# Performance work log

Measured on AMD Instinct MI355X. Metric: run time of the kernel, lower is better.

## Reference

```python
import jax, jax.numpy as jnp
import numpy as np

N_NODES, N_EDGES, N_GRAPHS = 50000, 600000, 64
SEQ_DIM, HID = 384, 128


def setup_inputs() -> dict:
    key = jax.random.key(0)
    ks = jax.random.split(key, 12)
    inp = {}
    inp["seq_emb"] = jax.random.normal(ks[0], (N_GRAPHS, SEQ_DIM), jnp.float32)
    inp["node_x"] = jax.random.normal(ks[1], (N_NODES, SEQ_DIM), jnp.float32)
    inp["edge_index"] = jax.random.randint(ks[2], (2, N_EDGES), 0, N_NODES, dtype=jnp.int32)
    inp["node_batch"] = jnp.sort(jax.random.randint(ks[3], (N_NODES,), 0, N_GRAPHS, dtype=jnp.int32))
    # learned parameters (fan-in scaled)
    inp["W1"] = jax.random.normal(ks[4], (SEQ_DIM, HID), jnp.float32) / np.sqrt(SEQ_DIM)
    inp["b1"] = jnp.zeros((HID,), jnp.float32)
    inp["W2"] = jax.random.normal(ks[5], (HID, HID), jnp.float32) / np.sqrt(HID)
    inp["b2"] = jnp.zeros((HID,), jnp.float32)
    inp["Wf"] = jax.random.normal(ks[6], (SEQ_DIM + HID, 128), jnp.float32) / np.sqrt(SEQ_DIM + HID)
    inp["bf"] = jnp.zeros((128,), jnp.float32)
    inp["Wtp"] = jax.random.normal(ks[7], (128, 2), jnp.float32) / np.sqrt(128)
    inp["btp"] = jnp.zeros((2,), jnp.float32)
    inp["Wp"] = jax.random.normal(ks[8], (128, 1), jnp.float32) / np.sqrt(128)
    inp["bp"] = jnp.zeros((1,), jnp.float32)
    return inp


def _gcn_conv(x, W, b, src, dst, norm, n_nodes):
    # PyG GCNConv: out = A_hat @ (x W) + b, A_hat = D^-1/2 (A+I) D^-1/2
    h = x @ W                                   # [N, H]
    msg = h[src] * norm[:, None]                # [E+N, H] gather + scale
    return jax.ops.segment_sum(msg, dst, num_segments=n_nodes) + b


def reference(seq_emb, node_x, edge_index, node_batch,
              W1, b1, W2, b2, Wf, bf, Wtp, btp, Wp, bp):
    n = node_x.shape[0]
    b_graphs = seq_emb.shape[0]
    loops = jnp.arange(n, dtype=edge_index.dtype)
    src = jnp.concatenate([edge_index[0], loops])
    dst = jnp.concatenate([edge_index[1], loops])
    # symmetric normalization with self-loops (deg >= 1)
    deg = jax.ops.segment_sum(jnp.ones_like(dst, dtype=node_x.dtype), dst, num_segments=n)
    dinv = deg ** -0.5
    norm = dinv[src] * dinv[dst]

    g = jax.nn.relu(_gcn_conv(node_x, W1, b1, src, dst, norm, n))
    g = jax.nn.relu(_gcn_conv(g, W2, b2, src, dst, norm, n))

    # global mean pool over graphs
    sums = jax.ops.segment_sum(g, node_batch, num_segments=b_graphs)
    cnts = jax.ops.segment_sum(jnp.ones((n,), g.dtype), node_batch, num_segments=b_graphs)
    pooled = sums / jnp.maximum(cnts, 1.0)[:, None]

    fused = jax.nn.relu(jnp.concatenate([seq_emb, pooled], axis=1) @ Wf + bf)
    tp_logits = fused @ Wtp + btp
    prom_pred = fused @ Wp + bp
    return (tp_logits, prom_pred)
```

## Files before the change

kernel.cpp:

```cpp
#include <hip/hip_runtime.h>


#define HID 128

typedef __attribute__((ext_vector_type(8))) short bf16x8;
typedef __attribute__((ext_vector_type(4))) short bf16x4;
typedef __attribute__((ext_vector_type(4))) float f32x4;

static __device__ __forceinline__ short f2bf(float f) {
  union { float f; unsigned u; } v; v.f = f;
  unsigned r = v.u + 0x7fff + ((v.u >> 16) & 1);
  return (short)(r >> 16);
}
static __device__ __forceinline__ float bf2f(short s) {
  union { unsigned u; float f; } v;
  v.u = ((unsigned)(unsigned short)s) << 16;
  return v.f;
}

__global__ __launch_bounds__(256) void prep_w_k(const float* __restrict__ W1,
                                                short* __restrict__ W1t,
                                                const float* __restrict__ W2,
                                                short* __restrict__ W2t,
                                                int* __restrict__ deg, int N) {
  int idx = blockIdx.x * 256 + threadIdx.x;
  if (idx < 384 * HID) {
    int k = idx >> 7;
    int c = idx & 127;
    W1t[(size_t)c * 384 + k] = f2bf(W1[idx]);
  } else if (idx < 384 * HID + HID * HID) {
    int j = idx - 384 * HID;
    int k = j >> 7;
    int c = j & 127;
    W2t[(size_t)c * HID + k] = f2bf(W2[j]);
  }
  if (idx < N) deg[idx] = 0;
}

__global__ __launch_bounds__(256) void hist_k(const int* __restrict__ dst,
                                              int* __restrict__ cnt, int E) {
  int i = blockIdx.x * 256 + threadIdx.x;
  if (i < E) atomicAdd(&cnt[dst[i]], 1);
}

__global__ __launch_bounds__(256) void scan_bsum(const int* __restrict__ cnt,
                                                 int* __restrict__ bsum,
                                                 float* __restrict__ dinv, int n) {
  __shared__ int sm[256];
  int i = blockIdx.x * 256 + threadIdx.x;
  int v = (i < n) ? cnt[i] : 0;
  if (i < n) dinv[i] = rsqrtf((float)(v + 1));
  sm[threadIdx.x] = v;
  __syncthreads();
  for (int off = 128; off > 0; off >>= 1) {
    if (threadIdx.x < off) sm[threadIdx.x] += sm[threadIdx.x + off];
    __syncthreads();
  }
  if (threadIdx.x == 0) bsum[blockIdx.x] = sm[0];
}

__global__ __launch_bounds__(256) void scan_offsets(const int* __restrict__ cnt,
                                                    const int* __restrict__ bsum,
                                                    int* __restrict__ offs,
                                                    int* __restrict__ cur,
                                                    float* __restrict__ sums,
                                                    int nsum, int n, int nb) {
  __shared__ int sm[256];
  int t = threadIdx.x;
  int bid = blockIdx.x;
  int zi = bid * 256 + t;
  if (zi < nsum) sums[zi] = 0.f;
  int bv = (t < nb) ? bsum[t] : 0;
  sm[t] = bv;
  __syncthreads();
  for (int off = 1; off < 256; off <<= 1) {
    int add = (t >= off) ? sm[t - off] : 0;
    __syncthreads();
    sm[t] += add;
    __syncthreads();
  }
  int base = (bid > 0) ? sm[bid - 1] : 0;
  __syncthreads();
  int i = bid * 256 + t;
  int v = (i < n) ? cnt[i] : 0;
  sm[t] = v;
  __syncthreads();
  for (int off = 1; off < 256; off <<= 1) {
    int add = (t >= off) ? sm[t - off] : 0;
    __syncthreads();
    sm[t] += add;
    __syncthreads();
  }
  if (i < n) {
    offs[i] = base + sm[t] - v;
    cur[i] = 0;
  }
  if (i == n - 1) offs[n] = base + sm[t];
}

__global__ __launch_bounds__(256) void fill_k(const int* __restrict__ src,
                                              const int* __restrict__ dst,
                                              const int* __restrict__ offs,
                                              int* __restrict__ cur,
                                              int* __restrict__ csr, int E) {
  int i = blockIdx.x * 256 + threadIdx.x;
  if (i >= E) return;
  int d = dst[i];
  int p = offs[d] + atomicAdd(&cur[d], 1);
  csr[p] = src[i];
}

__global__ __launch_bounds__(256) void mfma_gemm1_k(const float* __restrict__ Af,
                                                    const short* __restrict__ Wt,
                                                    const float* __restrict__ scale,
                                                    short* __restrict__ C, int M) {
  constexpr int K = 384;
  constexpr int BK = 64;
  constexpr int ROWE = BK + 8;
  __shared__ short As[64 * ROWE];
  __shared__ short Bs[128 * ROWE];
  __shared__ float dln[64];

  const int tid = threadIdx.x;
  const int wave = tid >> 6;
  const int lane = tid & 63;
  const int l15 = lane & 15;
  const int lk = lane >> 4;
  const int mh = (wave >> 1) * 32;
  const int nh = (wave & 1) * 64;
  const int row0 = blockIdx.x * 64;

  if (tid < 64) {
    int r = row0 + tid;
    dln[tid] = (r < M) ? scale[r] : 0.f;
  }

  f32x4 acc[2][4] = {};

  for (int k0 = 0; k0 < K; k0 += BK) {
    __syncthreads();
#pragma unroll
    for (int it = 0; it < 4; ++it) {
      int f = tid + it * 256;
      int r = f >> 4;
      int kc = (f & 15) << 2;
      int gr = row0 + r;
      float4 v = make_float4(0.f, 0.f, 0.f, 0.f);
      if (gr < M) v = *(const float4*)&Af[(size_t)gr * K + k0 + kc];
      bf16x4 s;
      s[0] = f2bf(v.x); s[1] = f2bf(v.y); s[2] = f2bf(v.z); s[3] = f2bf(v.w);
      *(bf16x4*)&As[r * ROWE + kc] = s;
    }
#pragma unroll
    for (int it = 0; it < 4; ++it) {
      int f = tid + it * 256;
      int r = f >> 3;
      int kc = (f & 7) << 3;
      *(bf16x8*)&Bs[r * ROWE + kc] =
          *(const bf16x8*)&Wt[(size_t)r * K + k0 + kc];
    }
    __syncthreads();
#pragma unroll
    for (int ks = 0; ks < 2; ++ks) {
      bf16x8 af[2], bfr[4];
#pragma unroll
      for (int mf = 0; mf < 2; ++mf)
        af[mf] = *(const bf16x8*)&As[(mh + mf * 16 + l15) * ROWE + ks * 32 + lk * 8];
#pragma unroll
      for (int nf = 0; nf < 4; ++nf)
        bfr[nf] = *(const bf16x8*)&Bs[(nh + nf * 16 + l15) * ROWE + ks * 32 + lk * 8];
#pragma unroll
      for (int mf = 0; mf < 2; ++mf)
#pragma unroll
        for (int nf = 0; nf < 4; ++nf)
          acc[mf][nf] = __builtin_amdgcn_mfma_f32_16x16x32_bf16(
              af[mf], bfr[nf], acc[mf][nf], 0, 0, 0);
    }
  }
#pragma unroll
  for (int mf = 0; mf < 2; ++mf) {
#pragma unroll
    for (int r = 0; r < 4; ++r) {
      int lr = mh + mf * 16 + lk * 4 + r;
      int gr = row0 + lr;
      if (gr >= M) continue;
      float s = dln[lr];
#pragma unroll
      for (int nf = 0; nf < 4; ++nf)
        C[(size_t)gr * HID + nh + nf * 16 + l15] = f2bf(acc[mf][nf][r] * s);
    }
  }
}

__global__ __launch_bounds__(256) void gemm2_agg_k(const short* __restrict__ Hs,
                                                   const int* __restrict__ offs,
                                                   const int* __restrict__ csr,
                                                   const float* __restrict__ dinv,
                                                   const float* __restrict__ b1,
                                                   const short* __restrict__ Wt,
                                                   short* __restrict__ C, int M) {
  constexpr int K = 128;
  constexpr int ROWE = K + 8;
  __shared__ short As[64 * ROWE];
  __shared__ short Bs[128 * ROWE];
  __shared__ float dln[64];

  const int tid = threadIdx.x;
  const int wave = tid >> 6;
  const int lane = tid & 63;
  const int l15 = lane & 15;
  const int lk = lane >> 4;
  const int mh = (wave >> 1) * 32;
  const int nh = (wave & 1) * 64;
  const int row0 = blockIdx.x * 64;

  if (tid < 64) {
    int r = row0 + tid;
    dln[tid] = (r < M) ? dinv[r] : 0.f;
  }

#pragma unroll
  for (int it = 0; it < 8; ++it) {
    int f = tid + it * 256;
    int r = f >> 4;
    int kc = (f & 15) << 3;
    *(bf16x8*)&Bs[r * ROWE + kc] = *(const bf16x8*)&Wt[(size_t)r * K + kc];
  }

  {
    const int srow = tid >> 2;
    const int sl = tid & 3;
    const int gr = row0 + srow;
    const int cb = sl * 32;
    float a[32];
#pragma unroll
    for (int q = 0; q < 32; ++q) a[q] = 0.f;
    if (gr < M) {
      int es = offs[gr];
      int ee = offs[gr + 1];
      float dvv = dinv[gr];
      const short* rs = &Hs[(size_t)gr * HID + cb];
#pragma unroll
      for (int h = 0; h < 4; ++h) {
        bf16x8 sv = *(const bf16x8*)(rs + h * 8);
#pragma unroll
        for (int q = 0; q < 8; ++q) a[h * 8 + q] = bf2f(sv[q]);
      }
      int p = es;
      for (; p + 4 <= ee; p += 4) {
        int u0 = __builtin_nontemporal_load(&csr[p + 0]);
        int u1 = __builtin_nontemporal_load(&csr[p + 1]);
        int u2 = __builtin_nontemporal_load(&csr[p + 2]);
        int u3 = __builtin_nontemporal_load(&csr[p + 3]);
        const short* r0 = &Hs[(size_t)u0 * HID + cb];
        const short* r1 = &Hs[(size_t)u1 * HID + cb];
        const short* r2 = &Hs[(size_t)u2 * HID + cb];
        const short* r3 = &Hs[(size_t)u3 * HID + cb];
#pragma unroll
        for (int h = 0; h < 4; ++h) {
          bf16x8 x0 = *(const bf16x8*)(r0 + h * 8);
          bf16x8 x1 = *(const bf16x8*)(r1 + h * 8);
          bf16x8 x2 = *(const bf16x8*)(r2 + h * 8);
          bf16x8 x3 = *(const bf16x8*)(r3 + h * 8);
#pragma unroll
          for (int q = 0; q < 8; ++q)
            a[h * 8 + q] += (bf2f(x0[q]) + bf2f(x1[q])) +
                            (bf2f(x2[q]) + bf2f(x3[q]));
        }
      }
      for (; p < ee; ++p) {
        int u = __builtin_nontemporal_load(&csr[p]);
        const short* r0 = &Hs[(size_t)u * HID + cb];
#pragma unroll
        for (int h = 0; h < 4; ++h) {
          bf16x8 x = *(const bf16x8*)(r0 + h * 8);
#pragma unroll
          for (int q = 0; q < 8; ++q) a[h * 8 + q] += bf2f(x[q]);
        }
      }
#pragma unroll
      for (int h = 0; h < 8; ++h) {
        float4 bb = *(const float4*)&b1[cb + h * 4];
        a[h * 4 + 0] = fmaxf(fmaf(a[h * 4 + 0], dvv, bb.x), 0.f);
        a[h * 4 + 1] = fmaxf(fmaf(a[h * 4 + 1], dvv, bb.y), 0.f);
        a[h * 4 + 2] = fmaxf(fmaf(a[h * 4 + 2], dvv, bb.z), 0.f);
        a[h * 4 + 3] = fmaxf(fmaf(a[h * 4 + 3], dvv, bb.w), 0.f);
      }
    }
#pragma unroll
    for (int h = 0; h < 4; ++h) {
      bf16x8 o;
#pragma unroll
      for (int q = 0; q < 8; ++q) o[q] = f2bf(a[h * 8 + q]);
      *(bf16x8*)&As[srow * ROWE + cb + h * 8] = o;
    }
  }
  __syncthreads();

  f32x4 acc[2][4] = {};
#pragma unroll
  for (int ks = 0; ks < 4; ++ks) {
    bf16x8 af[2], bfr[4];
#pragma unroll
    for (int mf = 0; mf < 2; ++mf)
      af[mf] = *(const bf16x8*)&As[(mh + mf * 16 + l15) * ROWE + ks * 32 + lk * 8];
#pragma unroll
    for (int nf = 0; nf < 4; ++nf)
      bfr[nf] = *(const bf16x8*)&Bs[(nh + nf * 16 + l15) * ROWE + ks * 32 + lk * 8];
#pragma unroll
    for (int mf = 0; mf < 2; ++mf)
#pragma unroll
      for (int nf = 0; nf < 4; ++nf)
        acc[mf][nf] = __builtin_amdgcn_mfma_f32_16x16x32_bf16(
            af[mf], bfr[nf], acc[mf][nf], 0, 0, 0);
  }
#pragma unroll
  for (int mf = 0; mf < 2; ++mf) {
#pragma unroll
    for (int r = 0; r < 4; ++r) {
      int lr = mh + mf * 16 + lk * 4 + r;
      int g2 = row0 + lr;
      if (g2 >= M) continue;
      float s = dln[lr];
#pragma unroll
      for (int nf = 0; nf < 4; ++nf)
        C[(size_t)g2 * HID + nh + nf * 16 + l15] = f2bf(acc[mf][nf][r] * s);
    }
  }
}

__global__ __launch_bounds__(512) void agg2_pool_k(const short* __restrict__ Hs,
                                                   const int* __restrict__ offs,
                                                   const int* __restrict__ csr,
                                                   const float* __restrict__ dinv,
                                                   const float* __restrict__ b2,
                                                   const int* __restrict__ batch,
                                                   float* __restrict__ sums,
                                                   int N) {
  const int nid = threadIdx.x >> 3;
  const int l8 = threadIdx.x & 7;
  const int v = blockIdx.x * 64 + nid;
  const int cb = l8 * 16;
  float a[16];
#pragma unroll
  for (int q = 0; q < 16; ++q) a[q] = 0.f;
  const bool valid = v < N;
  if (valid) {
    int es = offs[v];
    int ee = offs[v + 1];
    const short* rs = &Hs[(size_t)v * HID + cb];
    bf16x8 s0 = *(const bf16x8*)rs;
    bf16x8 s1 = *(const bf16x8*)(rs + 8);
#pragma unroll
    for (int q = 0; q < 8; ++q) { a[q] = bf2f(s0[q]); a[8 + q] = bf2f(s1[q]); }
    int p = es;
    for (; p + 8 <= ee; p += 8) {
      int u[8];
#pragma unroll
      for (int q = 0; q < 8; ++q) u[q] = __builtin_nontemporal_load(&csr[p + q]);
      bf16x8 xa[8], xb[8];
#pragma unroll
      for (int q = 0; q < 8; ++q) {
        const short* r0 = &Hs[(size_t)u[q] * HID + cb];
        xa[q] = *(const bf16x8*)r0;
        xb[q] = *(const bf16x8*)(r0 + 8);
      }
#pragma unroll
      for (int q = 0; q < 8; ++q)
#pragma unroll
        for (int r = 0; r < 8; ++r) {
          a[r] += bf2f(xa[q][r]);
          a[8 + r] += bf2f(xb[q][r]);
        }
    }
    for (; p + 4 <= ee; p += 4) {
      int u0 = __builtin_nontemporal_load(&csr[p + 0]);
      int u1 = __builtin_nontemporal_load(&csr[p + 1]);
      int u2 = __builtin_nontemporal_load(&csr[p + 2]);
      int u3 = __builtin_nontemporal_load(&csr[p + 3]);
      const short* r0 = &Hs[(size_t)u0 * HID + cb];
      const short* r1 = &Hs[(size_t)u1 * HID + cb];
      const short* r2 = &Hs[(size_t)u2 * HID + cb];
      const short* r3 = &Hs[(size_t)u3 * HID + cb];
      bf16x8 x0a = *(const bf16x8*)r0, x0b = *(const bf16x8*)(r0 + 8);
      bf16x8 x1a = *(const bf16x8*)r1, x1b = *(const bf16x8*)(r1 + 8);
      bf16x8 x2a = *(const bf16x8*)r2, x2b = *(const bf16x8*)(r2 + 8);
      bf16x8 x3a = *(const bf16x8*)r3, x3b = *(const bf16x8*)(r3 + 8);
#pragma unroll
      for (int q = 0; q < 8; ++q) {
        a[q]     += (bf2f(x0a[q]) + bf2f(x1a[q])) + (bf2f(x2a[q]) + bf2f(x3a[q]));
        a[8 + q] += (bf2f(x0b[q]) + bf2f(x1b[q])) + (bf2f(x2b[q]) + bf2f(x3b[q]));
      }
    }
    for (; p < ee; ++p) {
      int u = __builtin_nontemporal_load(&csr[p]);
      const short* r0 = &Hs[(size_t)u * HID + cb];
      bf16x8 xa = *(const bf16x8*)r0, xb = *(const bf16x8*)(r0 + 8);
#pragma unroll
      for (int q = 0; q < 8; ++q) { a[q] += bf2f(xa[q]); a[8 + q] += bf2f(xb[q]); }
    }
    float dv = dinv[v];
    float4 bb0 = *(const float4*)&b2[cb];
    float4 bb1 = *(const float4*)&b2[cb + 4];
    float4 bb2v = *(const float4*)&b2[cb + 8];
    float4 bb3 = *(const float4*)&b2[cb + 12];
    float bbv[16] = {bb0.x, bb0.y, bb0.z, bb0.w, bb1.x, bb1.y, bb1.z, bb1.w,
                     bb2v.x, bb2v.y, bb2v.z, bb2v.w, bb3.x, bb3.y, bb3.z, bb3.w};
#pragma unroll
    for (int q = 0; q < 16; ++q)
      a[q] = fmaxf(fmaf(a[q], dv, bbv[q]), 0.f);
  }
  __shared__ float ot[64 * 133];
  __shared__ int bsm[64];
#pragma unroll
  for (int q = 0; q < 16; ++q) ot[nid * 133 + cb + q] = a[q];
  if (threadIdx.x < 64) {
    int vv = blockIdx.x * 64 + threadIdx.x;
    bsm[threadIdx.x] = batch[vv < N ? vv : N - 1];
  }
  __syncthreads();
  int j = threadIdx.x & 127;
  int h = threadIdx.x >> 7;
  int r0 = h * 16;
  int g_cur = bsm[r0];
  float acc = 0.f;
#pragma unroll
  for (int rr = r0; rr < r0 + 16; ++rr) {
    int g = bsm[rr];
    if (g != g_cur) {
      atomicAdd(&sums[(size_t)g_cur * HID + j], acc);
      acc = 0.f;
      g_cur = g;
    }
    acc += ot[rr * 133 + j];
  }
  atomicAdd(&sums[(size_t)g_cur * HID + j], acc);
}

__global__ __launch_bounds__(128) void head_k(const float* __restrict__ seq,
                                              const float* __restrict__ sums,
                                              const int* __restrict__ batch,
                                              const float* __restrict__ Wf,
                                              const float* __restrict__ bf,
                                              const float* __restrict__ Wtp,
                                              const float* __restrict__ btp,
                                              const float* __restrict__ Wp,
                                              const float* __restrict__ bp,
                                              float* __restrict__ outp,
                                              int B, int SEQ, int n) {
  int g = blockIdx.x;
  int t = threadIdx.x;
  __shared__ float xin[512];
  __shared__ float fs[128];
  int lo = 0, hi = n;
  while (lo < hi) { int mid = (lo + hi) >> 1; if (batch[mid] < g) lo = mid + 1; else hi = mid; }
  int start = lo;
  hi = n;
  while (lo < hi) { int mid = (lo + hi) >> 1; if (batch[mid] <= g) lo = mid + 1; else hi = mid; }
  float inv_cnt = 1.f / fmaxf((float)(lo - start), 1.f);
  for (int i = t; i < SEQ; i += 128) xin[i] = seq[(size_t)g * SEQ + i];
  xin[SEQ + t] = sums[g * HID + t] * inv_cnt;
  __syncthreads();
  float acc = bf[t];
#pragma unroll 8
  for (int k = 0; k < 512; ++k) acc = fmaf(xin[k], Wf[(size_t)k * HID + t], acc);
  fs[t] = fmaxf(acc, 0.f);
  __syncthreads();
  if (t == 0) {
    float a0 = btp[0], a1 = btp[1], a2 = bp[0];
    for (int k = 0; k < 128; ++k) {
      float f = fs[k];
      a0 = fmaf(f, Wtp[k * 2 + 0], a0);
      a1 = fmaf(f, Wtp[k * 2 + 1], a1);
      a2 = fmaf(f, Wp[k], a2);
    }
    outp[g * 2 + 0] = a0;
    outp[g * 2 + 1] = a1;
    outp[B * 2 + g] = a2;
  }
}

extern "C" void kernel_launch(void* const* d_in, const int* in_sizes, int n_in,
                              void* d_out, int out_size, void* d_ws, size_t ws_size,
                              hipStream_t stream) {
  const float* seq_emb = (const float*)d_in[0];
  const float* node_x  = (const float*)d_in[1];
  const int*   eidx    = (const int*)d_in[2];
  const int*   nbatch  = (const int*)d_in[3];
  const float* W1  = (const float*)d_in[4];
  const float* b1  = (const float*)d_in[5];
  const float* W2  = (const float*)d_in[6];
  const float* b2  = (const float*)d_in[7];
  const float* Wf  = (const float*)d_in[8];
  const float* bfb = (const float*)d_in[9];
  const float* Wtp = (const float*)d_in[10];
  const float* btp = (const float*)d_in[11];
  const float* Wp  = (const float*)d_in[12];
  const float* bp  = (const float*)d_in[13];

  const int N = in_sizes[3];
  const int E = in_sizes[2] / 2;
  const int SEQ = 384;
  const int B = in_sizes[0] / SEQ;

  char* w = (char*)d_ws;
  auto alloc = [&](size_t bytes) -> void* {
    void* p = (void*)w;
    w += (bytes + 255) & ~(size_t)255;
    return p;
  };
  float* dinv   = (float*)alloc((size_t)N * 4);
  int*   deg    = (int*)alloc((size_t)N * 4);
  int*   cur    = (int*)alloc((size_t)N * 4);
  int*   offs   = (int*)alloc((size_t)(N + 1) * 4);
  int*   bsum   = (int*)alloc(1024);
  int*   csr    = (int*)alloc((size_t)E * 4);
  short* W1t    = (short*)alloc((size_t)SEQ * HID * 2);
  short* W2t    = (short*)alloc((size_t)HID * HID * 2);
  short* bufC   = (short*)alloc((size_t)N * HID * 2);
  short* bufD   = (short*)alloc((size_t)N * HID * 2);
  float* sums   = (float*)alloc((size_t)B * HID * 4);

  const int* srcp = eidx;
  const int* dstp = eidx + E;

  int gE = (E + 255) / 256;
  int gN = (N + 255) / 256;
  int wElems = SEQ * HID + HID * HID;
  int gP = (max(wElems, N) + 255) / 256;

  prep_w_k<<<gP, 256, 0, stream>>>(W1, W1t, W2, W2t, deg, N);
  hist_k<<<gE, 256, 0, stream>>>(dstp, deg, E);
  scan_bsum<<<gN, 256, 0, stream>>>(deg, bsum, dinv, N);
  scan_offsets<<<gN, 256, 0, stream>>>(deg, bsum, offs, cur, sums, B * HID, N, gN);
  fill_k<<<gE, 256, 0, stream>>>(srcp, dstp, offs, cur, csr, E);

  int gG = (N + 63) / 64;
  mfma_gemm1_k<<<gG, 256, 0, stream>>>(node_x, W1t, dinv, bufC, N);
  gemm2_agg_k<<<gG, 256, 0, stream>>>(bufC, offs, csr, dinv, b1, W2t, bufD, N);
  agg2_pool_k<<<gG, 512, 0, stream>>>(bufD, offs, csr, dinv, b2, nbatch, sums, N);
  head_k<<<B, 128, 0, stream>>>(seq_emb, sums, nbatch, Wf, bfb, Wtp, btp, Wp, bp,
                                (float*)d_out, B, SEQ, N);
}
```

Measured before the change: 210.1 us.

## Halve gemm2 weight LDS tile, drop nontemporal CSR loads, remove 8-way gather unroll

```diff
diff --git a/kernel.cpp b/kernel.cpp
--- a/kernel.cpp
+++ b/kernel.cpp
@@ -200,9 +200,10 @@
                                                    const short* __restrict__ Wt,
                                                    short* __restrict__ C, int M) {
   constexpr int K = 128;
-  constexpr int ROWE = K + 8;
-  __shared__ short As[64 * ROWE];
-  __shared__ short Bs[128 * ROWE];
+  constexpr int AROWE = K + 8;
+  constexpr int BROWE = 64 + 8;
+  __shared__ short As[64 * AROWE];
+  __shared__ short Bs[128 * BROWE];
   __shared__ float dln[64];
 
   const int tid = threadIdx.x;
@@ -220,11 +221,11 @@
   }
 
 #pragma unroll
-  for (int it = 0; it < 8; ++it) {
+  for (int it = 0; it < 4; ++it) {
     int f = tid + it * 256;
-    int r = f >> 4;
-    int kc = (f & 15) << 3;
-    *(bf16x8*)&Bs[r * ROWE + kc] = *(const bf16x8*)&Wt[(size_t)r * K + kc];
+    int r = f >> 3;
+    int kc = (f & 7) << 3;
+    *(bf16x8*)&Bs[r * BROWE + kc] = *(const bf16x8*)&Wt[(size_t)r * K + kc];
   }
 
   {
@@ -248,10 +249,10 @@
       }
       int p = es;
       for (; p + 4 <= ee; p += 4) {
-        int u0 = __builtin_nontemporal_load(&csr[p + 0]);
-        int u1 = __builtin_nontemporal_load(&csr[p + 1]);
-        int u2 = __builtin_nontemporal_load(&csr[p + 2]);
-        int u3 = __builtin_nontemporal_load(&csr[p + 3]);
+        int u0 = csr[p + 0];
+        int u1 = csr[p + 1];
+        int u2 = csr[p + 2];
+        int u3 = csr[p + 3];
         const short* r0 = &Hs[(size_t)u0 * HID + cb];
         const short* r1 = &Hs[(size_t)u1 * HID + cb];
         const short* r2 = &Hs[(size_t)u2 * HID + cb];
@@ -269,7 +270,7 @@
         }
       }
       for (; p < ee; ++p) {
-        int u = __builtin_nontemporal_load(&csr[p]);
+        int u = csr[p];
         const short* r0 = &Hs[(size_t)u * HID + cb];
 #pragma unroll
         for (int h = 0; h < 4; ++h) {
@@ -292,27 +293,44 @@
       bf16x8 o;
 #pragma unroll
       for (int q = 0; q < 8; ++q) o[q] = f2bf(a[h * 8 + q]);
-      *(bf16x8*)&As[srow * ROWE + cb + h * 8] = o;
+      *(bf16x8*)&As[srow * AROWE + cb + h * 8] = o;
     }
   }
   __syncthreads();
 
   f32x4 acc[2][4] = {};
 #pragma unroll
-  for (int ks = 0; ks < 4; ++ks) {
-    bf16x8 af[2], bfr[4];
-#pragma unroll
-    for (int mf = 0; mf < 2; ++mf)
-      af[mf] = *(const bf16x8*)&As[(mh + mf * 16 + l15) * ROWE + ks * 32 + lk * 8];
-#pragma unroll
-    for (int nf = 0; nf < 4; ++nf)
-      bfr[nf] = *(const bf16x8*)&Bs[(nh + nf * 16 + l15) * ROWE + ks * 32 + lk * 8];
-#pragma unroll
-    for (int mf = 0; mf < 2; ++mf)
+  for (int half = 0; half < 2; ++half) {
+    if (half == 1) {
+      __syncthreads();
+#pragma unroll
+      for (int it = 0; it < 4; ++it) {
+        int f = tid + it * 256;
+        int r = f >> 3;
+        int kc = (f & 7) << 3;
+        *(bf16x8*)&Bs[r * BROWE + kc] =
+            *(const bf16x8*)&Wt[(size_t)r * K + 64 + kc];
+      }
+      __syncthreads();
+    }
+#pragma unroll
+    for (int ks = 0; ks < 2; ++ks) {
+      bf16x8 af[2], bfr[4];
+#pragma unroll
+      for (int mf = 0; mf < 2; ++mf)
+        af[mf] = *(const bf16x8*)
+            &As[(mh + mf * 16 + l15) * AROWE + half * 64 + ks * 32 + lk * 8];
 #pragma unroll
       for (int nf = 0; nf < 4; ++nf)
-        acc[mf][nf] = __builtin_amdgcn_mfma_f32_16x16x32_bf16(
-            af[mf], bfr[nf], acc[mf][nf], 0, 0, 0);
+        bfr[nf] = *(const bf16x8*)
+            &Bs[(nh + nf * 16 + l15) * BROWE + ks * 32 + lk * 8];
+#pragma unroll
+      for (int mf = 0; mf < 2; ++mf)
+#pragma unroll
+        for (int nf = 0; nf < 4; ++nf)
+          acc[mf][nf] = __builtin_amdgcn_mfma_f32_16x16x32_bf16(
+              af[mf], bfr[nf], acc[mf][nf], 0, 0, 0);
+    }
   }
 #pragma unroll
   for (int mf = 0; mf < 2; ++mf) {
@@ -354,30 +372,11 @@
 #pragma unroll
     for (int q = 0; q < 8; ++q) { a[q] = bf2f(s0[q]); a[8 + q] = bf2f(s1[q]); }
     int p = es;
-    for (; p + 8 <= ee; p += 8) {
-      int u[8];
-#pragma unroll
-      for (int q = 0; q < 8; ++q) u[q] = __builtin_nontemporal_load(&csr[p + q]);
-      bf16x8 xa[8], xb[8];
-#pragma unroll
-      for (int q = 0; q < 8; ++q) {
-        const short* r0 = &Hs[(size_t)u[q] * HID + cb];
-        xa[q] = *(const bf16x8*)r0;
-        xb[q] = *(const bf16x8*)(r0 + 8);
-      }
-#pragma unroll
-      for (int q = 0; q < 8; ++q)
-#pragma unroll
-        for (int r = 0; r < 8; ++r) {
-          a[r] += bf2f(xa[q][r]);
-          a[8 + r] += bf2f(xb[q][r]);
-        }
-    }
     for (; p + 4 <= ee; p += 4) {
-      int u0 = __builtin_nontemporal_load(&csr[p + 0]);
-      int u1 = __builtin_nontemporal_load(&csr[p + 1]);
-      int u2 = __builtin_nontemporal_load(&csr[p + 2]);
-      int u3 = __builtin_nontemporal_load(&csr[p + 3]);
+      int u0 = csr[p + 0];
+      int u1 = csr[p + 1];
+      int u2 = csr[p + 2];
+      int u3 = csr[p + 3];
       const short* r0 = &Hs[(size_t)u0 * HID + cb];
       const short* r1 = &Hs[(size_t)u1 * HID + cb];
       const short* r2 = &Hs[(size_t)u2 * HID + cb];
@@ -393,7 +392,7 @@
       }
     }
     for (; p < ee; ++p) {
-      int u = __builtin_nontemporal_load(&csr[p]);
+      int u = csr[p];
       const short* r0 = &Hs[(size_t)u * HID + cb];
       bf16x8 xa = *(const bf16x8*)r0, xb = *(const bf16x8*)(r0 + 8);
 #pragma unroll
```

Result: no change. 208.3 us (-0.8%).
